# Optimization experiments

Hardware: AMD Instinct MI355X
Metric: run time of the kernel (lower is better)

## Reference

```python
import jax, jax.numpy as jnp
import numpy as np

B, S = 128, 64          # batch, sequence length (cities)
H = 128                 # hidden size
STATIC, DYNAMIC = 2, 2  # static/dynamic feature channels


def setup_inputs() -> dict:
    key = jax.random.key(0)
    ks = jax.random.split(key, 16)
    g = lambda k, shape: (jax.random.normal(k, shape, dtype=jnp.float32) * 0.1)
    return {
        "static": jax.random.normal(ks[0], (B, STATIC, S), dtype=jnp.float32),
        "dynamic": jax.random.uniform(ks[1], (B, DYNAMIC, S), dtype=jnp.float32),
        "x0": jnp.zeros((STATIC,), jnp.float32),           # learned initial decoder input
        "static_w": g(ks[2], (H, STATIC)),  "static_b": g(ks[3], (H,)),
        "dynamic_w": g(ks[4], (H, DYNAMIC)), "dynamic_b": g(ks[5], (H,)),
        "decoder_w": g(ks[6], (H, STATIC)), "decoder_b": g(ks[7], (H,)),
        "gru_wih": g(ks[8], (3 * H, H)), "gru_whh": g(ks[9], (3 * H, H)),
        "gru_bih": g(ks[10], (3 * H,)), "gru_bhh": g(ks[11], (3 * H,)),
        "attn_v": g(ks[12], (H,)), "attn_W": g(ks[13], (H, 3 * H)),
        "ptr_v": g(ks[14], (H,)),  "ptr_W": g(ks[15], (H, 2 * H)),
    }


def _forward(static, dynamic, x0, static_w, static_b, dynamic_w, dynamic_b,
             decoder_w, decoder_b, gru_wih, gru_whh, gru_bih, gru_bhh,
             attn_v, attn_W, ptr_v, ptr_W):
    Bsz, in_size, seq = static.shape
    # Conv1d with kernel_size=1 == pointwise channel mixing
    conv = lambda w, b, x: jnp.einsum('oi,bis->bos', w, x) + b[None, :, None]
    static_h = conv(static_w, static_b, static)      # [B,H,S]
    dynamic_h = conv(dynamic_w, dynamic_b, dynamic)  # [B,H,S]

    def gru_cell(x, h):
        # torch nn.GRU gate order: r, z, n
        gi = x @ gru_wih.T + gru_bih
        gh = h @ gru_whh.T + gru_bhh
        i_r, i_z, i_n = jnp.split(gi, 3, axis=1)
        h_r, h_z, h_n = jnp.split(gh, 3, axis=1)
        r = jax.nn.sigmoid(i_r + h_r)
        z = jax.nn.sigmoid(i_z + h_z)
        n = jnp.tanh(i_n + r * h_n)
        return (1.0 - z) * n + z * h

    def step(carry, _):
        dec_in, h = carry                                   # [B,in,1], [B,H]
        dec_h = conv(decoder_w, decoder_b, dec_in)[:, :, 0]  # [B,H]
        h_new = gru_cell(dec_h, h)                           # rnn_out == last_hh (1 layer)
        rnn_out = h_new
        # encoder attention over cities
        hid = jnp.concatenate(
            [static_h, dynamic_h,
             jnp.broadcast_to(rnn_out[:, :, None], static_h.shape)], axis=1)  # [B,3H,S]
        e = jnp.tanh(jnp.einsum('hk,bks->bhs', attn_W, hid))
        attns = jax.nn.softmax(jnp.einsum('h,bhs->bs', attn_v, e), axis=1)    # [B,S]
        context = jnp.einsum('bs,bhs->bh', attns, static_h)                   # [B,H]
        energy = jnp.concatenate(
            [static_h, jnp.broadcast_to(context[:, :, None], static_h.shape)], axis=1)
        logits = jnp.einsum('h,bhs->bs', ptr_v,
                            jnp.tanh(jnp.einsum('hk,bks->bhs', ptr_W, energy)))
        # mask_fn is None -> mask stays all ones -> mask.log() == 0
        logp_all = jax.nn.log_softmax(logits, axis=1)
        ptr = jnp.argmax(logp_all, axis=1)                  # greedy (eval mode)
        logp = jnp.take_along_axis(logp_all, ptr[:, None], axis=1)[:, 0]
        idx = jnp.broadcast_to(ptr[:, None, None], (Bsz, in_size, 1))
        new_in = jax.lax.stop_gradient(jnp.take_along_axis(static, idx, axis=2))
        return (new_in, h_new), (ptr, logp)

    dec0 = jnp.broadcast_to(x0[None, :, None], (Bsz, in_size, 1))
    h0 = jnp.zeros((Bsz, static_h.shape[1]), static.dtype)
    _, (ptrs, logps) = jax.lax.scan(step, (dec0, h0), None, length=seq)
    return ptrs.T, logps.T  # tour_idx [B,S] int, tour_logp [B,S] float


def reference(static, dynamic, x0, static_w, static_b, dynamic_w, dynamic_b,
              decoder_w, decoder_b, gru_wih, gru_whh, gru_bih, gru_bhh,
              attn_v, attn_W, ptr_v, ptr_W):
    return _forward(static, dynamic, x0, static_w, static_b, dynamic_w, dynamic_b,
                    decoder_w, decoder_b, gru_wih, gru_whh, gru_bih, gru_bhh,
                    attn_v, attn_W, ptr_v, ptr_W)
```

## Files before the change

kernel.cpp:

```cpp
#include <hip/hip_runtime.h>
#include <math.h>


#define K1  1.44269504088896340736f
#define K2  2.88539008177792681472f
#define LN2 0.69314718055994530942f

#define WS_M     0
#define WS_C     768
#define WS_PREA  1152
#define WS_PREP  (WS_PREA + 128*8192)
#define WS_Q     (WS_PREP + 128*8192)

template <int CTRL>
__device__ __forceinline__ float dppf(float x) {
  int xi = __builtin_bit_cast(int, x);
  return __builtin_bit_cast(float,
      __builtin_amdgcn_update_dpp(xi, xi, CTRL, 0xF, 0xF, false));
}
__device__ __forceinline__ float sum4(float x) {
  x += dppf<0xB1>(x); x += dppf<0x4E>(x); return x;
}
__device__ __forceinline__ float sum8(float x) {
  x += dppf<0xB1>(x); x += dppf<0x4E>(x); x += dppf<0x141>(x); return x;
}
__device__ __forceinline__ float sum16(float x) {
  x += dppf<0xB1>(x); x += dppf<0x4E>(x); x += dppf<0x141>(x); x += dppf<0x128>(x);
  return x;
}
__device__ __forceinline__ float sum64(float x) {
  x = sum16(x); x += __shfl_xor(x, 16); x += __shfl_xor(x, 32); return x;
}
__device__ __forceinline__ float max64(float x) {
  x = fmaxf(x, dppf<0xB1>(x)); x = fmaxf(x, dppf<0x4E>(x));
  x = fmaxf(x, dppf<0x141>(x)); x = fmaxf(x, dppf<0x128>(x));
  x = fmaxf(x, __shfl_xor(x, 16)); x = fmaxf(x, __shfl_xor(x, 32)); return x;
}
#define RCP(x)  __builtin_amdgcn_rcpf(x)
#define EXP2(x) __builtin_amdgcn_exp2f(x)

__device__ __forceinline__ int rot8(int p) {
  return (p & 56) | ((p + (p >> 3)) & 7);
}

__global__ __launch_bounds__(256) void prep_small(
    const float* __restrict__ wih, const float* __restrict__ decw,
    const float* __restrict__ decb, const float* __restrict__ bih,
    float* __restrict__ ws) {
  int gid = blockIdx.x * 256 + threadIdx.x;
  if (gid < 384) {
    float m0 = 0.f, m1 = 0.f, cc = 0.f;
    for (int k = 0; k < 128; ++k) {
      float w = wih[gid * 128 + k];
      m0 += w * decw[k * 2 + 0];
      m1 += w * decw[k * 2 + 1];
      cc += w * decb[k];
    }
    ws[WS_M + gid * 2 + 0] = m0;
    ws[WS_M + gid * 2 + 1] = m1;
    ws[WS_C + gid] = cc + bih[gid];
  }
}

__global__ __launch_bounds__(256) void prep_big(
    const float* __restrict__ statics, const float* __restrict__ dynamics,
    const float* __restrict__ sw, const float* __restrict__ sb,
    const float* __restrict__ dw, const float* __restrict__ db,
    const float* __restrict__ attn_W, const float* __restrict__ ptr_W,
    float* __restrict__ ws) {
  __shared__ __align__(16) float sh[128 * 64];
  __shared__ __align__(16) float dh[128 * 64];
  __shared__ float st[128];
  __shared__ float dy[128];
  int b = blockIdx.x >> 3;
  int hq = blockIdx.x & 7;
  int t = threadIdx.x;
  if (t < 128) st[t] = statics[b * 128 + t];
  else         dy[t - 128] = dynamics[b * 128 + (t - 128)];
  __syncthreads();
  for (int e = t; e < 8192; e += 256) {
    int h = e >> 6, s = e & 63;
    sh[e] = sw[h * 2 + 0] * st[s] + sw[h * 2 + 1] * st[64 + s] + sb[h];
    dh[e] = dw[h * 2 + 0] * dy[s] + dw[h * 2 + 1] * dy[64 + s] + db[h];
  }
  __syncthreads();
  int hh = hq * 16 + (t >> 4);
  int s0 = (t & 15) * 4;
  float4 pA = {0, 0, 0, 0}, pP = {0, 0, 0, 0}, qq = {0, 0, 0, 0};
  for (int k = 0; k < 128; ++k) {
    float4 sv = *(const float4*)&sh[k * 64 + s0];
    float4 dv = *(const float4*)&dh[k * 64 + s0];
    float w1 = attn_W[hh * 384 + k];
    float w2 = attn_W[hh * 384 + 128 + k];
    float p1 = ptr_W[hh * 256 + k];
    float p2 = ptr_W[hh * 256 + 128 + k];
    pA.x += w1 * sv.x + w2 * dv.x;  pA.y += w1 * sv.y + w2 * dv.y;
    pA.z += w1 * sv.z + w2 * dv.z;  pA.w += w1 * sv.w + w2 * dv.w;
    pP.x += p1 * sv.x;  pP.y += p1 * sv.y;  pP.z += p1 * sv.z;  pP.w += p1 * sv.w;
    qq.x += p2 * sv.x;  qq.y += p2 * sv.y;  qq.z += p2 * sv.z;  qq.w += p2 * sv.w;
  }
  float4 eA, eP;
  eA.x = exp2f(K2 * pA.x); eA.y = exp2f(K2 * pA.y);
  eA.z = exp2f(K2 * pA.z); eA.w = exp2f(K2 * pA.w);
  eP.x = exp2f(K2 * pP.x); eP.y = exp2f(K2 * pP.y);
  eP.z = exp2f(K2 * pP.z); eP.w = exp2f(K2 * pP.w);
  int o = b * 8192 + hh * 64 + s0;
  *(float4*)&ws[WS_PREA + o] = eA;
  *(float4*)&ws[WS_PREP + o] = eP;
  *(float4*)&ws[WS_Q + o]    = qq;
}

__global__ __launch_bounds__(512)
__attribute__((amdgpu_waves_per_eu(2)))
void drl4tsp_main(
    const float* __restrict__ statics, const float* __restrict__ x0,
    const float* __restrict__ whh, const float* __restrict__ attn_W,
    const float* __restrict__ bhh_g, const float* __restrict__ attn_v,
    const float* __restrict__ ptr_v, const float* __restrict__ ws,
    float* __restrict__ out) {
  __shared__ float4 W3s4[128 * 32];
  __shared__ float4 EAT4[64 * 32];
  __shared__ float4 EPT4[64 * 32];
  __shared__ float4 uav3[64];
  __shared__ float4 uav2[64];
  __shared__ float4 gp4[128 * 3];
  __shared__ __align__(16) float hp[144];
  __shared__ __align__(16) float attns[64];
  __shared__ float a_lds[64];
  __shared__ float l_lds[64];
  __shared__ float stt[128];

  const int b    = blockIdx.x;
  const int t    = threadIdx.x;
  const int lane = t & 63;
  const int g    = t >> 2;
  const int q    = t & 3;
  const int s    = t >> 3;
  const int hg   = t & 7;

  float wr0[32], wr1[32], wr2[32];
#pragma unroll
  for (int kk = 0; kk < 8; ++kk) {
    float4 a = *(const float4*)(whh + g * 128         + kk * 16 + q * 4);
    float4 c = *(const float4*)(whh + (128 + g) * 128 + kk * 16 + q * 4);
    float4 d = *(const float4*)(whh + (256 + g) * 128 + kk * 16 + q * 4);
    wr0[4*kk] = a.x; wr0[4*kk+1] = a.y; wr0[4*kk+2] = a.z; wr0[4*kk+3] = a.w;
    wr1[4*kk] = c.x; wr1[4*kk+1] = c.y; wr1[4*kk+2] = c.z; wr1[4*kk+3] = c.w;
    wr2[4*kk] = d.x; wr2[4*kk+1] = d.y; wr2[4*kk+2] = d.z; wr2[4*kk+3] = d.w;
  }
  float qr[16];
  {
    const float4* pq = (const float4*)(ws + WS_Q + b * 8192 + g * 64 + q * 16);
#pragma unroll
    for (int i = 0; i < 4; ++i) {
      float4 v = pq[i];
      qr[4*i] = v.x; qr[4*i+1] = v.y; qr[4*i+2] = v.z; qr[4*i+3] = v.w;
    }
  }

  {
    const float4* src = (const float4*)(attn_W + g * 384 + 256);
#pragma unroll
    for (int kk = 0; kk < 8; ++kk) {
      int j = q * 8 + kk;
      W3s4[g * 32 + ((j + g) & 31)] = src[j];
    }
  }
  for (int e = t; e < 8192; e += 512) {
    int h = e >> 6, sE = e & 63;
    int rg = ((h >> 2) + sE) & 31;
    ((float*)EAT4)[sE * 128 + rg * 4 + (h & 3)] = ws[WS_PREA + b * 8192 + e];
    ((float*)EPT4)[sE * 128 + rg * 4 + (h & 3)] = ws[WS_PREP + b * 8192 + e];
  }
  if (t < 128) {
    int h = t;
    int rg = rot8(h >> 1);
    ((float*)uav3)[rg * 4 + (h & 1) * 2 + 1] = 2.0f * attn_v[h];
    ((float*)uav2)[rg * 4 + (h & 1) * 2 + 1] = 2.0f * ptr_v[h];
    stt[h] = statics[b * 128 + h];
    const float* Mm = ws + WS_M;
    const float* Cc = ws + WS_C;
    float cR = Cc[h] + bhh_g[h];
    float cZ = Cc[128 + h] + bhh_g[128 + h];
    gp4[h*3 + 0] = float4{Mm[h*2], Mm[h*2+1], cR, Mm[(128+h)*2]};
    gp4[h*3 + 1] = float4{Mm[(128+h)*2+1], cZ, Mm[(256+h)*2], Mm[(256+h)*2+1]};
    gp4[h*3 + 2] = float4{Cc[256+h], bhh_g[256+h], 0.f, 0.f};
  }
  __syncthreads();

  float hreg = 0.f, ghr = 0.f, ghz = 0.f, ghn = 0.f;
  float d0 = x0[0], d1 = x0[1];

  for (int step = 0; step < 64; ++step) {
    {
      float4 v0 = gp4[g*3], v1 = gp4[g*3+1], v2 = gp4[g*3+2];
      float r = RCP(1.f + EXP2(-K1 * (v0.x*d0 + v0.y*d1 + v0.z + ghr)));
      float z = RCP(1.f + EXP2(-K1 * (v0.w*d0 + v1.x*d1 + v1.y + ghz)));
      float xn = v1.z*d0 + v1.w*d1 + v2.x + r * (ghn + v2.y);
      float n = 1.f - 2.f * RCP(EXP2(K2 * xn) + 1.f);
      hreg = (1.f - z) * n + z * hreg;
      if (q == 0) hp[(g >> 5) * 36 + (g & 31)] = hreg;
    }
    __syncthreads();
    {
      float u3a = 0.f, u3b = 0.f;
#pragma unroll
      for (int kk = 0; kk < 8; ++kk) {
        float4 hv = *(const float4*)&hp[(kk >> 1) * 36 + (kk & 1) * 16 + q * 4];
        float4 wv = W3s4[g * 32 + ((kk * 4 + q + g) & 31)];
        float d2 = wv.x*hv.x + wv.y*hv.y + wv.z*hv.z + wv.w*hv.w;
        if (kk & 1) u3b += d2; else u3a += d2;
      }
      float u3 = sum4(u3a + u3b);
      if (q == 0)
        ((float*)uav3)[rot8(g >> 1) * 4 + (g & 1) * 2] = EXP2(K2 * u3);
    }
    __syncthreads();
    float sr = 0.f, sz = 0.f, sn = 0.f;
    {
      float acc0 = 0.f, acc1 = 0.f;
#pragma unroll
      for (int ii = 0; ii < 4; ++ii) {
        float4 ea = EAT4[s * 32 + ((hg * 4 + ii + s) & 31)];
        int p0 = hg * 8 + 2 * ii;
        float4 ua = uav3[(p0 & 56) | ((p0 + hg) & 7)];
        float4 ub = uav3[((p0+1) & 56) | ((p0 + 1 + hg) & 7)];
        acc0 += ua.y * RCP(ea.x * ua.x + 1.f)
              + ua.w * RCP(ea.y * ua.z + 1.f);
        acc1 += ub.y * RCP(ea.z * ub.x + 1.f)
              + ub.w * RCP(ea.w * ub.z + 1.f);
      }
#pragma unroll
      for (int kk = 0; kk < 4; ++kk) {
        float4 hv = *(const float4*)&hp[(kk >> 1) * 36 + (kk & 1) * 16 + q * 4];
        int k = kk * 4;
        sr += wr0[k]*hv.x + wr0[k+1]*hv.y + wr0[k+2]*hv.z + wr0[k+3]*hv.w;
        sz += wr1[k]*hv.x + wr1[k+1]*hv.y + wr1[k+2]*hv.z + wr1[k+3]*hv.w;
        sn += wr2[k]*hv.x + wr2[k+1]*hv.y + wr2[k+2]*hv.z + wr2[k+3]*hv.w;
      }
      float acc = sum8(acc0 + acc1);
      if (hg == 0) a_lds[s] = -acc;
    }
    __syncthreads();
    {
      float a = a_lds[lane];
      float e = EXP2(K1 * a);
      attns[lane] = e;
#pragma unroll
      for (int kk = 4; kk < 8; ++kk) {
        float4 hv = *(const float4*)&hp[(kk >> 1) * 36 + (kk & 1) * 16 + q * 4];
        int k = kk * 4;
        sr += wr0[k]*hv.x + wr0[k+1]*hv.y + wr0[k+2]*hv.z + wr0[k+3]*hv.w;
        sz += wr1[k]*hv.x + wr1[k+1]*hv.y + wr1[k+2]*hv.z + wr1[k+3]*hv.w;
        sn += wr2[k]*hv.x + wr2[k+1]*hv.y + wr2[k+2]*hv.z + wr2[k+3]*hv.w;
      }
      float sum = sum64(e);
      float p = 0.f;
#pragma unroll
      for (int ii = 0; ii < 4; ++ii) {
        float4 av = *(const float4*)&attns[q * 16 + ii * 4];
        p += qr[4*ii]*av.x + qr[4*ii+1]*av.y + qr[4*ii+2]*av.z + qr[4*ii+3]*av.w;
      }
      p *= RCP(sum);
      p = sum4(p);
      if (q == 0)
        ((float*)uav2)[rot8(g >> 1) * 4 + (g & 1) * 2] = EXP2(K2 * p);
      ghr = sum4(sr); ghz = sum4(sz); ghn = sum4(sn);
    }
    __syncthreads();
    {
      float acc0 = 0.f, acc1 = 0.f;
#pragma unroll
      for (int ii = 0; ii < 4; ++ii) {
        float4 ep = EPT4[s * 32 + ((hg * 4 + ii + s) & 31)];
        int p0 = hg * 8 + 2 * ii;
        float4 ua = uav2[(p0 & 56) | ((p0 + hg) & 7)];
        float4 ub = uav2[((p0+1) & 56) | ((p0 + 1 + hg) & 7)];
        acc0 += ua.y * RCP(ep.x * ua.x + 1.f)
              + ua.w * RCP(ep.y * ua.z + 1.f);
        acc1 += ub.y * RCP(ep.z * ub.x + 1.f)
              + ub.w * RCP(ep.w * ub.z + 1.f);
      }
      float acc = sum8(acc0 + acc1);
      if (hg == 0) l_lds[s] = -acc;
    }
    __syncthreads();
    {
      float L = l_lds[lane];
      float v = max64(L);
      unsigned long long mk = __ballot(L == v);
      int idx = __builtin_ctzll(mk);
      float e2 = EXP2(K1 * (L - v));
      float s3 = sum64(e2);
      if (t == 0) {
        out[b * 64 + step] = (float)idx;
        out[8192 + b * 64 + step] = -LN2 * __builtin_amdgcn_logf(s3);
      }
      d0 = stt[idx];
      d1 = stt[64 + idx];
    }
  }
}

extern "C" void kernel_launch(void* const* d_in, const int* in_sizes, int n_in,
                              void* d_out, int out_size, void* d_ws, size_t ws_size,
                              hipStream_t stream) {
  const float* statics  = (const float*)d_in[0];
  const float* dynamics = (const float*)d_in[1];
  const float* x0       = (const float*)d_in[2];
  const float* sw       = (const float*)d_in[3];
  const float* sb       = (const float*)d_in[4];
  const float* dw       = (const float*)d_in[5];
  const float* db       = (const float*)d_in[6];
  const float* decw     = (const float*)d_in[7];
  const float* decb     = (const float*)d_in[8];
  const float* wih      = (const float*)d_in[9];
  const float* whh      = (const float*)d_in[10];
  const float* bih      = (const float*)d_in[11];
  const float* bhh      = (const float*)d_in[12];
  const float* attn_v   = (const float*)d_in[13];
  const float* attn_W   = (const float*)d_in[14];
  const float* ptr_v    = (const float*)d_in[15];
  const float* ptr_W    = (const float*)d_in[16];
  float* ws  = (float*)d_ws;
  float* out = (float*)d_out;

  hipLaunchKernelGGL(prep_small, dim3(2), dim3(256), 0, stream,
                     wih, decw, decb, bih, ws);
  hipLaunchKernelGGL(prep_big, dim3(1024), dim3(256), 0, stream,
                     statics, dynamics, sw, sb, dw, db, attn_W, ptr_W, ws);
  hipLaunchKernelGGL(drl4tsp_main, dim3(128), dim3(512), 0, stream,
                     statics, x0, whh, attn_W, bhh, attn_v, ptr_v, ws, out);
}
```

Measured before the change: 217.5 us.

## Use LDS-only barriers, merge reciprocals, prefetch EPT and buffer outputs in LDS

Replaces __syncthreads with a barrier that waits only on LDS counters, so per-step global stores no longer stall the barrier. It also buffers the per-step outputs in shared memory and writes them once after the loop. Pairs of reciprocals in the attention and pointer sums are merged into one RCP of a product, which halves transcendental ops but risks overflow or precision loss. It also prefetches the EPT rows before the preceding barrier to hide LDS latency.

```diff
diff --git a/kernel.cpp b/kernel.cpp
--- a/kernel.cpp
+++ b/kernel.cpp
@@ -38,6 +38,12 @@
 }
 #define RCP(x)  __builtin_amdgcn_rcpf(x)
 #define EXP2(x) __builtin_amdgcn_exp2f(x)
+
+__device__ __forceinline__ void bar_lds() {
+  asm volatile("s_waitcnt lgkmcnt(0)" ::: "memory");
+  __builtin_amdgcn_s_barrier();
+  asm volatile("" ::: "memory");
+}
 
 __device__ __forceinline__ int rot8(int p) {
   return (p & 56) | ((p + (p >> 3)) & 7);
@@ -129,6 +135,7 @@
   __shared__ float a_lds[64];
   __shared__ float l_lds[64];
   __shared__ float stt[128];
+  __shared__ float outbuf[128];
 
   const int b    = blockIdx.x;
   const int t    = threadIdx.x;
@@ -201,7 +208,7 @@
       hreg = (1.f - z) * n + z * hreg;
       if (q == 0) hp[(g >> 5) * 36 + (g & 31)] = hreg;
     }
-    __syncthreads();
+    bar_lds();
     {
       float u3a = 0.f, u3b = 0.f;
 #pragma unroll
@@ -215,7 +222,7 @@
       if (q == 0)
         ((float*)uav3)[rot8(g >> 1) * 4 + (g & 1) * 2] = EXP2(K2 * u3);
     }
-    __syncthreads();
+    bar_lds();
     float sr = 0.f, sz = 0.f, sn = 0.f;
     {
       float acc0 = 0.f, acc1 = 0.f;
@@ -225,10 +232,10 @@
         int p0 = hg * 8 + 2 * ii;
         float4 ua = uav3[(p0 & 56) | ((p0 + hg) & 7)];
         float4 ub = uav3[((p0+1) & 56) | ((p0 + 1 + hg) & 7)];
-        acc0 += ua.y * RCP(ea.x * ua.x + 1.f)
-              + ua.w * RCP(ea.y * ua.z + 1.f);
-        acc1 += ub.y * RCP(ea.z * ub.x + 1.f)
-              + ub.w * RCP(ea.w * ub.z + 1.f);
+        float x1 = ea.x * ua.x + 1.f, y1 = ea.y * ua.z + 1.f;
+        acc0 += (ua.y * y1 + ua.w * x1) * RCP(x1 * y1);
+        float x2 = ea.z * ub.x + 1.f, y2 = ea.w * ub.z + 1.f;
+        acc1 += (ub.y * y2 + ub.w * x2) * RCP(x2 * y2);
       }
 #pragma unroll
       for (int kk = 0; kk < 4; ++kk) {
@@ -241,9 +248,14 @@
       float acc = sum8(acc0 + acc1);
       if (hg == 0) a_lds[s] = -acc;
     }
-    __syncthreads();
+    bar_lds();
+    float4 ep0, ep1, ep2, ep3;
     {
       float a = a_lds[lane];
+      ep0 = EPT4[s * 32 + ((hg * 4 + 0 + s) & 31)];
+      ep1 = EPT4[s * 32 + ((hg * 4 + 1 + s) & 31)];
+      ep2 = EPT4[s * 32 + ((hg * 4 + 2 + s) & 31)];
+      ep3 = EPT4[s * 32 + ((hg * 4 + 3 + s) & 31)];
       float e = EXP2(K1 * a);
       attns[lane] = e;
 #pragma unroll
@@ -267,24 +279,24 @@
         ((float*)uav2)[rot8(g >> 1) * 4 + (g & 1) * 2] = EXP2(K2 * p);
       ghr = sum4(sr); ghz = sum4(sz); ghn = sum4(sn);
     }
-    __syncthreads();
+    bar_lds();
     {
       float acc0 = 0.f, acc1 = 0.f;
 #pragma unroll
       for (int ii = 0; ii < 4; ++ii) {
-        float4 ep = EPT4[s * 32 + ((hg * 4 + ii + s) & 31)];
+        float4 ep = (ii == 0) ? ep0 : (ii == 1) ? ep1 : (ii == 2) ? ep2 : ep3;
         int p0 = hg * 8 + 2 * ii;
         float4 ua = uav2[(p0 & 56) | ((p0 + hg) & 7)];
         float4 ub = uav2[((p0+1) & 56) | ((p0 + 1 + hg) & 7)];
-        acc0 += ua.y * RCP(ep.x * ua.x + 1.f)
-              + ua.w * RCP(ep.y * ua.z + 1.f);
-        acc1 += ub.y * RCP(ep.z * ub.x + 1.f)
-              + ub.w * RCP(ep.w * ub.z + 1.f);
+        float x1 = ep.x * ua.x + 1.f, y1 = ep.y * ua.z + 1.f;
+        acc0 += (ua.y * y1 + ua.w * x1) * RCP(x1 * y1);
+        float x2 = ep.z * ub.x + 1.f, y2 = ep.w * ub.z + 1.f;
+        acc1 += (ub.y * y2 + ub.w * x2) * RCP(x2 * y2);
       }
       float acc = sum8(acc0 + acc1);
       if (hg == 0) l_lds[s] = -acc;
     }
-    __syncthreads();
+    bar_lds();
     {
       float L = l_lds[lane];
       float v = max64(L);
@@ -293,13 +305,16 @@
       float e2 = EXP2(K1 * (L - v));
       float s3 = sum64(e2);
       if (t == 0) {
-        out[b * 64 + step] = (float)idx;
-        out[8192 + b * 64 + step] = -LN2 * __builtin_amdgcn_logf(s3);
+        outbuf[step] = (float)idx;
+        outbuf[64 + step] = -LN2 * __builtin_amdgcn_logf(s3);
       }
       d0 = stt[idx];
       d1 = stt[64 + idx];
     }
   }
+  bar_lds();
+  if (t < 64)        out[b * 64 + t]         = outbuf[t];
+  else if (t < 128)  out[8192 + b * 64 + (t - 64)] = outbuf[t];
 }
 
 extern "C" void kernel_launch(void* const* d_in, const int* in_sizes, int n_in,
```

New measurement: 205.4 us. 5.6% less time.
